# Kernel tuning notes

Measured on AMD Instinct MI355X. Metric: run time of the kernel, lower is better.

Reference implementation:

```python
import jax, jax.numpy as jnp
import numpy as np

# --- module constants (match init_kwargs) ---
DIM = 256
WH, WW = 8, 8            # window_size
H, W = 64, 64            # input_resolution
NUM_HEADS = 1
HEAD_DIM = DIM // NUM_HEADS
SCALE = HEAD_DIM ** -0.5
N = WH * WW
TAB_P = 2 * WW - 1       # a_p/b_p table size (input_resolution != window_size)
TAB_R = 2 * WH - 1


def _relative_coords():
    ch, cw = np.meshgrid(np.arange(WH), np.arange(WW), indexing='ij')
    flat = np.stack([ch.reshape(-1), cw.reshape(-1)])          # (2, N)
    rel = flat[:, :, None] - flat[:, None, :]                  # (2, N, N)
    radius = rel[0]                                            # (N, N) in [-(WH-1), WH-1]
    azimuth = rel[1]                                           # (N, N) in [-(WW-1), WW-1]
    return jnp.asarray(radius, jnp.int32), jnp.asarray(azimuth, jnp.int32)


def setup_inputs() -> dict:
    key = jax.random.key(0)
    ks = jax.random.split(key, 12)
    B_ = 2048
    std = 0.02
    return {
        'x': jax.random.normal(ks[0], (B_, N, DIM), jnp.float32),
        'theta_max': jax.random.uniform(ks[1], (WH,), jnp.float32),
        'qkv_w': jax.random.normal(ks[2], (3 * DIM, DIM), jnp.float32) * (DIM ** -0.5),
        'qkv_b': jnp.zeros((3 * DIM,), jnp.float32),
        'proj_w': jax.random.normal(ks[3], (DIM, DIM), jnp.float32) * (DIM ** -0.5),
        'proj_b': jnp.zeros((DIM,), jnp.float32),
        'a_p': jax.random.normal(ks[4], (TAB_P, NUM_HEADS), jnp.float32) * std,
        'b_p': jax.random.normal(ks[5], (TAB_P, NUM_HEADS), jnp.float32) * std,
        'a_r': jax.random.normal(ks[6], (TAB_R, NUM_HEADS), jnp.float32) * std,
        'b_r': jax.random.normal(ks[7], (TAB_R, NUM_HEADS), jnp.float32) * std,
    }


def reference(x, theta_max, qkv_w, qkv_b, proj_w, proj_b, a_p, b_p, a_r, b_r):
    radius, azimuth = _relative_coords()
    # phi: gather azimuth table (negative indices wrap like torch) + trig bias
    az_idx = jnp.mod(azimuth, TAB_P)
    az_ang = (azimuth.astype(x.dtype) * (2.0 * np.pi / W))[:, :, None]      # (N,N,1)
    A_phi = a_p[az_idx] * jnp.cos(az_ang) + b_p[az_idx] * jnp.sin(az_ang)   # (N,N,h)
    # theta: gather radius table + per-row theta_max scaled trig bias
    r_idx = jnp.mod(radius, TAB_R)
    time_t = N // theta_max.shape[0]
    tmax = jnp.repeat(theta_max, time_t)                                    # (N,)
    r_ang = (radius.astype(x.dtype) * tmax / H)[:, :, None]                 # (N,N,1)
    A_theta = a_r[r_idx] * jnp.cos(r_ang) + b_r[r_idx] * jnp.sin(r_ang)     # (N,N,h)
    bias = jnp.transpose(A_phi + A_theta, (2, 0, 1))[None]                  # (1,h,N,N)

    B_ = x.shape[0]
    qkv = x @ qkv_w.T + qkv_b                                               # (B_,N,3*DIM)
    qkv = qkv.reshape(B_, N, 3, NUM_HEADS, HEAD_DIM).transpose(2, 0, 3, 1, 4)
    q, k, v = qkv[0], qkv[1], qkv[2]                                        # (B_,h,N,hd)
    attn = jnp.einsum('bhnd,bhmd->bhnm', q * SCALE, k) + bias
    attn = jax.nn.softmax(attn, axis=-1)
    out = jnp.einsum('bhnm,bhmd->bhnd', attn, v)                            # (B_,h,N,hd)
    out = out.transpose(0, 2, 1, 3).reshape(B_, N, DIM)
    return out @ proj_w.T + proj_b
```

## Files before the change

### kernel.cpp

```cpp
#include <hip/hip_runtime.h>
#include <hip/hip_bf16.h>


typedef __bf16 bf16x8_t __attribute__((ext_vector_type(8)));
typedef __bf16 bf16x4_t __attribute__((ext_vector_type(4)));
typedef float floatx4_t __attribute__((ext_vector_type(4)));

#define MFMA16(a, b, c) __builtin_amdgcn_mfma_f32_16x16x32_bf16(a, b, c, 0, 0, 0)
#define VPITCH 72

__device__ __forceinline__ void cvt8(const float* src, __bf16* dst) {
  float4 f0 = reinterpret_cast<const float4*>(src)[0];
  float4 f1 = reinterpret_cast<const float4*>(src)[1];
  bf16x8_t h;
  h[0] = (__bf16)f0.x; h[1] = (__bf16)f0.y; h[2] = (__bf16)f0.z; h[3] = (__bf16)f0.w;
  h[4] = (__bf16)f1.x; h[5] = (__bf16)f1.y; h[6] = (__bf16)f1.z; h[7] = (__bf16)f1.w;
  *reinterpret_cast<bf16x8_t*>(dst) = h;
}

__global__ __launch_bounds__(256) void prep_kernel(
    const float* __restrict__ qkv_w, const float* __restrict__ qkv_b,
    const float* __restrict__ proj_w, const float* __restrict__ theta_max,
    const float* __restrict__ a_p, const float* __restrict__ b_p,
    const float* __restrict__ a_r, const float* __restrict__ b_r,
    __bf16* __restrict__ wb, float* __restrict__ bias_ws,
    float* __restrict__ btl) {
  int blk = blockIdx.x, tid = threadIdx.x;
  if (blk < 64) {
    int t = blk * 256 + tid;
    cvt8(&qkv_w[(size_t)t * 8], &wb[(size_t)t * 8]);
  } else if (blk < 80) {
    int t = (blk - 64) * 256 + tid;
    int i = t >> 6, j = t & 63;
    int rad = (i >> 3) - (j >> 3), az = (i & 7) - (j & 7);
    int azm = ((az % 15) + 15) % 15;
    int rdm = ((rad % 15) + 15) % 15;
    float az_ang = (float)az * 0.09817477042468103f;
    float tm = theta_max[j >> 3];
    float r_ang = (float)rad * tm * (1.0f / 64.0f);
    bias_ws[t] = a_p[azm] * cosf(az_ang) + b_p[azm] * sinf(az_ang) +
                 a_r[rdm] * cosf(r_ang) + b_r[rdm] * sinf(r_ang);
  } else {
    int j = blk - 80;
    int k = tid;
    float s = 0.f;
    for (int d = 0; d < 256; ++d)
      s += proj_w[j * 256 + d] * qkv_w[(size_t)(512 + d) * 256 + k];
    wb[(size_t)(512 + j) * 256 + k] = (__bf16)s;
    if (tid == 0) {
      float sb = 0.f;
      for (int d = 0; d < 256; ++d) sb += proj_w[j * 256 + d] * qkv_b[512 + d];
      btl[j] = sb;
    }
  }
}

__global__ __launch_bounds__(256, 1) void fused_kernel(
    const float* __restrict__ x, const __bf16* __restrict__ wb,
    const float* __restrict__ qkv_b, const float* __restrict__ btl,
    const float* __restrict__ bias_ws, const float* __restrict__ proj_b,
    float* __restrict__ out) {
  __shared__ __align__(16) __bf16 ldsX[64 * 256];
  __shared__ __align__(16) __bf16 ldsQ[64 * 256];
  __shared__ __align__(16) __bf16 ldsK[64 * 256];
  __shared__ __align__(16) __bf16 ldsV[256 * 64];
  __shared__ __align__(16) __bf16 ldsP[64 * VPITCH];
  const int b = blockIdx.x;
  const size_t xbase = (size_t)b * 64 * 256;
  const int tid = threadIdx.x;
  const int lane = tid & 63, wave = tid >> 6;
  const int l15 = lane & 15, quad = lane >> 4;

  {
    int m = tid >> 2;
    int u0 = tid & 3;
#pragma unroll
    for (int i = 0; i < 8; ++i) {
      int u = u0 + i * 4;
      __bf16 tmp[8];
      cvt8(&x[xbase + m * 256 + u * 8], tmp);
      *reinterpret_cast<bf16x8_t*>(&ldsX[(m * 32 + (u ^ (m & 7))) * 8]) =
          *reinterpret_cast<bf16x8_t*>(tmp);
    }
  }
  __syncthreads();

#pragma unroll 1
  for (int p = 0; p < 3; ++p) {
    floatx4_t acc[4][4] = {};
#pragma unroll
    for (int kc = 0; kc < 8; ++kc) {
      bf16x8_t af[4], bfr[4];
#pragma unroll
      for (int mt = 0; mt < 4; ++mt)
        af[mt] = *reinterpret_cast<const bf16x8_t*>(
            &ldsX[((mt * 16 + l15) * 32 + ((kc * 4 + quad) ^ (l15 & 7))) * 8]);
#pragma unroll
      for (int ct = 0; ct < 4; ++ct) {
        int n = p * 256 + wave * 64 + ct * 16 + l15;
        bfr[ct] = *reinterpret_cast<const bf16x8_t*>(
            &wb[(size_t)n * 256 + kc * 32 + quad * 8]);
      }
#pragma unroll
      for (int mt = 0; mt < 4; ++mt)
#pragma unroll
        for (int ct = 0; ct < 4; ++ct)
          acc[mt][ct] = MFMA16(af[mt], bfr[ct], acc[mt][ct]);
    }
    if (p < 2) {
      __bf16* dst = (p == 0) ? ldsQ : ldsK;
#pragma unroll
      for (int ct = 0; ct < 4; ++ct) {
        int d = wave * 64 + ct * 16 + l15;
        float bias = qkv_b[p * 256 + d];
        int u = d >> 3;
#pragma unroll
        for (int mt = 0; mt < 4; ++mt)
#pragma unroll
          for (int g = 0; g < 4; ++g) {
            int m = mt * 16 + quad * 4 + g;
            dst[(m * 32 + (u ^ (m & 7))) * 8 + (d & 7)] =
                (__bf16)(acc[mt][ct][g] + bias);
          }
      }
    } else {
#pragma unroll
      for (int ct = 0; ct < 4; ++ct) {
        int d = wave * 64 + ct * 16 + l15;
        float bias = btl[d];
#pragma unroll
        for (int mt = 0; mt < 4; ++mt) {
          bf16x4_t pk;
#pragma unroll
          for (int g = 0; g < 4; ++g) pk[g] = (__bf16)(acc[mt][ct][g] + bias);
          int u = mt * 2 + (quad >> 1);
          *reinterpret_cast<bf16x4_t*>(
              &ldsV[(d * 8 + (u ^ (d & 7))) * 8 + (quad & 1) * 4]) = pk;
        }
      }
    }
    __syncthreads();
  }

  bf16x8_t qf[8];
#pragma unroll
  for (int kc = 0; kc < 8; ++kc)
    qf[kc] = *reinterpret_cast<const bf16x8_t*>(
        &ldsQ[((wave * 16 + l15) * 32 + ((kc * 4 + quad) ^ (l15 & 7))) * 8]);

  floatx4_t accs[4] = {};
#pragma unroll
  for (int ct = 0; ct < 4; ++ct)
#pragma unroll
    for (int kc = 0; kc < 8; ++kc) {
      bf16x8_t bfr = *reinterpret_cast<const bf16x8_t*>(
          &ldsK[((ct * 16 + l15) * 32 + ((kc * 4 + quad) ^ (l15 & 7))) * 8]);
      accs[ct] = MFMA16(qf[kc], bfr, accs[ct]);
    }

  float p[4][4];
#pragma unroll
  for (int ct = 0; ct < 4; ++ct)
#pragma unroll
    for (int g = 0; g < 4; ++g) {
      int row = wave * 16 + quad * 4 + g;
      p[ct][g] = accs[ct][g] * 0.0625f + bias_ws[row * 64 + ct * 16 + l15];
    }
#pragma unroll
  for (int g = 0; g < 4; ++g) {
    float m = fmaxf(fmaxf(p[0][g], p[1][g]), fmaxf(p[2][g], p[3][g]));
#pragma unroll
    for (int off = 1; off < 16; off <<= 1) m = fmaxf(m, __shfl_xor(m, off, 64));
    float l = 0.f;
#pragma unroll
    for (int ct = 0; ct < 4; ++ct) {
      p[ct][g] = __expf(p[ct][g] - m);
      l += p[ct][g];
    }
#pragma unroll
    for (int off = 1; off < 16; off <<= 1) l += __shfl_xor(l, off, 64);
    float inv = 1.0f / l;
    int row = wave * 16 + quad * 4 + g;
#pragma unroll
    for (int ct = 0; ct < 4; ++ct)
      ldsP[row * VPITCH + ct * 16 + l15] = (__bf16)(p[ct][g] * inv);
  }
  __syncthreads();

  floatx4_t acco[16] = {};
#pragma unroll
  for (int kc = 0; kc < 2; ++kc) {
    bf16x8_t af = *reinterpret_cast<const bf16x8_t*>(
        &ldsP[(wave * 16 + l15) * VPITCH + kc * 32 + quad * 8]);
#pragma unroll
    for (int ct = 0; ct < 16; ++ct) {
      int n = ct * 16 + l15;
      bf16x8_t bfr = *reinterpret_cast<const bf16x8_t*>(
          &ldsV[(n * 8 + ((kc * 4 + quad) ^ (n & 7))) * 8]);
      acco[ct] = MFMA16(af, bfr, acco[ct]);
    }
  }

#pragma unroll
  for (int ct = 0; ct < 16; ++ct) {
    int col = ct * 16 + l15;
    float pbv = proj_b[col];
#pragma unroll
    for (int g = 0; g < 4; ++g) {
      int row = wave * 16 + quad * 4 + g;
      out[xbase + (size_t)row * 256 + col] = acco[ct][g] + pbv;
    }
  }
}

extern "C" void kernel_launch(void* const* d_in, const int* in_sizes, int n_in,
                              void* d_out, int out_size, void* d_ws, size_t ws_size,
                              hipStream_t stream) {
  const float* x = (const float*)d_in[0];
  const float* theta_max = (const float*)d_in[1];
  const float* qkv_w = (const float*)d_in[2];
  const float* qkv_b = (const float*)d_in[3];
  const float* proj_w = (const float*)d_in[4];
  const float* proj_b = (const float*)d_in[5];
  const float* a_p = (const float*)d_in[6];
  const float* b_p = (const float*)d_in[7];
  const float* a_r = (const float*)d_in[8];
  const float* b_r = (const float*)d_in[9];
  float* out = (float*)d_out;

  char* ws = (char*)d_ws;
  float* bias_ws = (float*)ws;
  float* btl = (float*)(ws + 16384);
  __bf16* wb = (__bf16*)(ws + 32768);

  hipLaunchKernelGGL(prep_kernel, dim3(336), dim3(256), 0, stream,
                     qkv_w, qkv_b, proj_w, theta_max, a_p, b_p, a_r, b_r,
                     wb, bias_ws, btl);
  hipLaunchKernelGGL(fused_kernel, dim3(2048), dim3(256), 0, stream,
                     x, wb, qkv_b, btl, bias_ws, proj_b, out);
}
```

Measured before the change: 409.9 us.

## Fold Wq^T Wk into single matrix for scores and cut LDS for two blocks per CU

Precomputes M = Wq^T Wk (scaled) plus a key-bias column, so the scores become X·M·X^T instead of separate Q and K projections. The per-window K projection and its LDS buffer are removed, and the V buffer is aliased onto the G buffer. This lowers shared memory enough to allow two blocks per CU via launch bounds. The trade-off is a larger prep kernel, an extra small GEMM against X, and slightly different bf16 rounding. Softmax is also reorganised so each lane owns one query row.

```diff
diff --git a/kernel.cpp b/kernel.cpp
--- a/kernel.cpp
+++ b/kernel.cpp
@@ -23,14 +23,35 @@
     const float* __restrict__ proj_w, const float* __restrict__ theta_max,
     const float* __restrict__ a_p, const float* __restrict__ b_p,
     const float* __restrict__ a_r, const float* __restrict__ b_r,
-    __bf16* __restrict__ wb, float* __restrict__ bias_ws,
-    float* __restrict__ btl) {
+    __bf16* __restrict__ wbM, __bf16* __restrict__ wbV,
+    float* __restrict__ bias_ws, float* __restrict__ btl) {
   int blk = blockIdx.x, tid = threadIdx.x;
-  if (blk < 64) {
-    int t = blk * 256 + tid;
-    cvt8(&qkv_w[(size_t)t * 8], &wb[(size_t)t * 8]);
-  } else if (blk < 80) {
-    int t = (blk - 64) * 256 + tid;
+  if (blk < 256) {
+    int n = blk, k = tid;
+    float s = 0.f;
+    for (int a = 0; a < 256; ++a)
+      s += qkv_w[(size_t)a * 256 + k] * qkv_w[(size_t)(256 + a) * 256 + n];
+    wbM[(size_t)n * 256 + k] = (__bf16)(s * 0.0625f);
+  } else if (blk == 256) {
+    int k = tid;
+    float s = 0.f;
+    for (int a = 0; a < 256; ++a)
+      s += qkv_w[(size_t)(256 + a) * 256 + k] * qkv_b[a];
+    wbM[(size_t)256 * 256 + k] = (__bf16)(s * 0.0625f);
+    for (int r = 257; r < 272; ++r) wbM[(size_t)r * 256 + k] = (__bf16)0.f;
+  } else if (blk < 513) {
+    int j = blk - 257, k = tid;
+    float s = 0.f;
+    for (int d = 0; d < 256; ++d)
+      s += proj_w[j * 256 + d] * qkv_w[(size_t)(512 + d) * 256 + k];
+    wbV[(size_t)j * 256 + k] = (__bf16)s;
+    if (tid == 0) {
+      float sb = 0.f;
+      for (int d = 0; d < 256; ++d) sb += proj_w[j * 256 + d] * qkv_b[512 + d];
+      btl[j] = sb;
+    }
+  } else {
+    int t = (blk - 513) * 256 + tid;
     int i = t >> 6, j = t & 63;
     int rad = (i >> 3) - (j >> 3), az = (i & 7) - (j & 7);
     int azm = ((az % 15) + 15) % 15;
@@ -40,30 +61,16 @@
     float r_ang = (float)rad * tm * (1.0f / 64.0f);
     bias_ws[t] = a_p[azm] * cosf(az_ang) + b_p[azm] * sinf(az_ang) +
                  a_r[rdm] * cosf(r_ang) + b_r[rdm] * sinf(r_ang);
-  } else {
-    int j = blk - 80;
-    int k = tid;
-    float s = 0.f;
-    for (int d = 0; d < 256; ++d)
-      s += proj_w[j * 256 + d] * qkv_w[(size_t)(512 + d) * 256 + k];
-    wb[(size_t)(512 + j) * 256 + k] = (__bf16)s;
-    if (tid == 0) {
-      float sb = 0.f;
-      for (int d = 0; d < 256; ++d) sb += proj_w[j * 256 + d] * qkv_b[512 + d];
-      btl[j] = sb;
-    }
-  }
-}
-
-__global__ __launch_bounds__(256, 1) void fused_kernel(
-    const float* __restrict__ x, const __bf16* __restrict__ wb,
-    const float* __restrict__ qkv_b, const float* __restrict__ btl,
+  }
+}
+
+__global__ __launch_bounds__(256, 2) void fused_kernel(
+    const float* __restrict__ x, const __bf16* __restrict__ wbM,
+    const __bf16* __restrict__ wbV, const float* __restrict__ btl,
     const float* __restrict__ bias_ws, const float* __restrict__ proj_b,
     float* __restrict__ out) {
-  __shared__ __align__(16) __bf16 ldsX[64 * 256];
-  __shared__ __align__(16) __bf16 ldsQ[64 * 256];
-  __shared__ __align__(16) __bf16 ldsK[64 * 256];
-  __shared__ __align__(16) __bf16 ldsV[256 * 64];
+  __shared__ __align__(16) __bf16 ldsX[64 * 32 * 8];
+  __shared__ __align__(16) __bf16 ldsG[64 * 34 * 8];
   __shared__ __align__(16) __bf16 ldsP[64 * VPITCH];
   const int b = blockIdx.x;
   const size_t xbase = (size_t)b * 64 * 256;
@@ -85,9 +92,9 @@
   }
   __syncthreads();
 
-#pragma unroll 1
-  for (int p = 0; p < 3; ++p) {
-    floatx4_t acc[4][4] = {};
+  {
+    floatx4_t accg[4][4] = {};
+    floatx4_t accc[4] = {};
 #pragma unroll
     for (int kc = 0; kc < 8; ++kc) {
       bf16x8_t af[4], bfr[4];
@@ -97,118 +104,163 @@
             &ldsX[((mt * 16 + l15) * 32 + ((kc * 4 + quad) ^ (l15 & 7))) * 8]);
 #pragma unroll
       for (int ct = 0; ct < 4; ++ct) {
-        int n = p * 256 + wave * 64 + ct * 16 + l15;
+        int n = (ct * 4 + wave) * 16 + l15;
         bfr[ct] = *reinterpret_cast<const bf16x8_t*>(
-            &wb[(size_t)n * 256 + kc * 32 + quad * 8]);
+            &wbM[(size_t)n * 256 + kc * 32 + quad * 8]);
       }
 #pragma unroll
       for (int mt = 0; mt < 4; ++mt)
 #pragma unroll
         for (int ct = 0; ct < 4; ++ct)
-          acc[mt][ct] = MFMA16(af[mt], bfr[ct], acc[mt][ct]);
-    }
-    if (p < 2) {
-      __bf16* dst = (p == 0) ? ldsQ : ldsK;
+          accg[mt][ct] = MFMA16(af[mt], bfr[ct], accg[mt][ct]);
+      if (wave == 0) {
+        bf16x8_t bc = *reinterpret_cast<const bf16x8_t*>(
+            &wbM[(size_t)(256 + l15) * 256 + kc * 32 + quad * 8]);
+#pragma unroll
+        for (int mt = 0; mt < 4; ++mt) accc[mt] = MFMA16(af[mt], bc, accc[mt]);
+      }
+    }
+#pragma unroll
+    for (int ct = 0; ct < 4; ++ct) {
+      int n0 = (ct * 4 + wave) * 16 + l15;
+      int u = n0 >> 3;
+#pragma unroll
+      for (int mt = 0; mt < 4; ++mt)
+#pragma unroll
+        for (int g = 0; g < 4; ++g) {
+          int m = mt * 16 + quad * 4 + g;
+          ldsG[(m * 34 + (u ^ (m & 7))) * 8 + (n0 & 7)] =
+              (__bf16)accg[mt][ct][g];
+        }
+    }
+    if (wave == 0) {
+      int n0 = 256 + l15;
+      int u = 32 + (l15 >> 3);
+#pragma unroll
+      for (int mt = 0; mt < 4; ++mt)
+#pragma unroll
+        for (int g = 0; g < 4; ++g) {
+          int m = mt * 16 + quad * 4 + g;
+          ldsG[(m * 34 + u) * 8 + (n0 & 7)] = (__bf16)accc[mt][g];
+        }
+    }
+  }
+  __syncthreads();
+
+  floatx4_t accs[4] = {};
+#pragma unroll
+  for (int kc = 0; kc < 8; ++kc) {
+    bf16x8_t af[4];
+#pragma unroll
+    for (int mt = 0; mt < 4; ++mt)
+      af[mt] = *reinterpret_cast<const bf16x8_t*>(
+          &ldsX[((mt * 16 + l15) * 32 + ((kc * 4 + quad) ^ (l15 & 7))) * 8]);
+    int r = wave * 16 + l15;
+    bf16x8_t bfr = *reinterpret_cast<const bf16x8_t*>(
+        &ldsG[(r * 34 + ((kc * 4 + quad) ^ (r & 7))) * 8]);
+#pragma unroll
+    for (int mt = 0; mt < 4; ++mt) accs[mt] = MFMA16(af[mt], bfr, accs[mt]);
+  }
+
+  {
+    const int i = wave * 16 + l15;
+    float p[4][4];
+    float mx = -1e30f;
+#pragma unroll
+    for (int mt = 0; mt < 4; ++mt)
+#pragma unroll
+      for (int g = 0; g < 4; ++g) {
+        int j = mt * 16 + quad * 4 + g;
+        float cj = (float)ldsG[(j * 34 + 32) * 8];
+        p[mt][g] = accs[mt][g] + bias_ws[i * 64 + j] + cj;
+        mx = fmaxf(mx, p[mt][g]);
+      }
+    mx = fmaxf(mx, __shfl_xor(mx, 16, 64));
+    mx = fmaxf(mx, __shfl_xor(mx, 32, 64));
+    float l = 0.f;
+#pragma unroll
+    for (int mt = 0; mt < 4; ++mt)
+#pragma unroll
+      for (int g = 0; g < 4; ++g) {
+        p[mt][g] = __expf(p[mt][g] - mx);
+        l += p[mt][g];
+      }
+    l += __shfl_xor(l, 16, 64);
+    l += __shfl_xor(l, 32, 64);
+    float inv = 1.0f / l;
+#pragma unroll
+    for (int mt = 0; mt < 4; ++mt)
+#pragma unroll
+      for (int g = 0; g < 4; ++g) {
+        int j = mt * 16 + quad * 4 + g;
+        ldsP[i * VPITCH + j] = (__bf16)(p[mt][g] * inv);
+      }
+  }
+  __syncthreads();
+
+  {
+    __bf16* ldsV = ldsG;
+    floatx4_t accv[4][4] = {};
+#pragma unroll
+    for (int kc = 0; kc < 8; ++kc) {
+      bf16x8_t af[4], bfr[4];
+#pragma unroll
+      for (int mt = 0; mt < 4; ++mt)
+        af[mt] = *reinterpret_cast<const bf16x8_t*>(
+            &ldsX[((mt * 16 + l15) * 32 + ((kc * 4 + quad) ^ (l15 & 7))) * 8]);
 #pragma unroll
       for (int ct = 0; ct < 4; ++ct) {
-        int d = wave * 64 + ct * 16 + l15;
-        float bias = qkv_b[p * 256 + d];
-        int u = d >> 3;
-#pragma unroll
-        for (int mt = 0; mt < 4; ++mt)
-#pragma unroll
-          for (int g = 0; g < 4; ++g) {
-            int m = mt * 16 + quad * 4 + g;
-            dst[(m * 32 + (u ^ (m & 7))) * 8 + (d & 7)] =
-                (__bf16)(acc[mt][ct][g] + bias);
-          }
-      }
-    } else {
-#pragma unroll
-      for (int ct = 0; ct < 4; ++ct) {
-        int d = wave * 64 + ct * 16 + l15;
-        float bias = btl[d];
-#pragma unroll
-        for (int mt = 0; mt < 4; ++mt) {
-          bf16x4_t pk;
-#pragma unroll
-          for (int g = 0; g < 4; ++g) pk[g] = (__bf16)(acc[mt][ct][g] + bias);
-          int u = mt * 2 + (quad >> 1);
-          *reinterpret_cast<bf16x4_t*>(
-              &ldsV[(d * 8 + (u ^ (d & 7))) * 8 + (quad & 1) * 4]) = pk;
-        }
-      }
-    }
-    __syncthreads();
-  }
-
-  bf16x8_t qf[8];
-#pragma unroll
-  for (int kc = 0; kc < 8; ++kc)
-    qf[kc] = *reinterpret_cast<const bf16x8_t*>(
-        &ldsQ[((wave * 16 + l15) * 32 + ((kc * 4 + quad) ^ (l15 & 7))) * 8]);
-
-  floatx4_t accs[4] = {};
-#pragma unroll
-  for (int ct = 0; ct < 4; ++ct)
-#pragma unroll
-    for (int kc = 0; kc < 8; ++kc) {
-      bf16x8_t bfr = *reinterpret_cast<const bf16x8_t*>(
-          &ldsK[((ct * 16 + l15) * 32 + ((kc * 4 + quad) ^ (l15 & 7))) * 8]);
-      accs[ct] = MFMA16(qf[kc], bfr, accs[ct]);
-    }
-
-  float p[4][4];
-#pragma unroll
-  for (int ct = 0; ct < 4; ++ct)
-#pragma unroll
-    for (int g = 0; g < 4; ++g) {
-      int row = wave * 16 + quad * 4 + g;
-      p[ct][g] = accs[ct][g] * 0.0625f + bias_ws[row * 64 + ct * 16 + l15];
-    }
-#pragma unroll
-  for (int g = 0; g < 4; ++g) {
-    float m = fmaxf(fmaxf(p[0][g], p[1][g]), fmaxf(p[2][g], p[3][g]));
-#pragma unroll
-    for (int off = 1; off < 16; off <<= 1) m = fmaxf(m, __shfl_xor(m, off, 64));
-    float l = 0.f;
+        int n = wave * 64 + ct * 16 + l15;
+        bfr[ct] = *reinterpret_cast<const bf16x8_t*>(
+            &wbV[(size_t)n * 256 + kc * 32 + quad * 8]);
+      }
+#pragma unroll
+      for (int mt = 0; mt < 4; ++mt)
+#pragma unroll
+        for (int ct = 0; ct < 4; ++ct)
+          accv[mt][ct] = MFMA16(af[mt], bfr[ct], accv[mt][ct]);
+    }
 #pragma unroll
     for (int ct = 0; ct < 4; ++ct) {
-      p[ct][g] = __expf(p[ct][g] - m);
-      l += p[ct][g];
-    }
-#pragma unroll
-    for (int off = 1; off < 16; off <<= 1) l += __shfl_xor(l, off, 64);
-    float inv = 1.0f / l;
-    int row = wave * 16 + quad * 4 + g;
-#pragma unroll
-    for (int ct = 0; ct < 4; ++ct)
-      ldsP[row * VPITCH + ct * 16 + l15] = (__bf16)(p[ct][g] * inv);
-  }
-  __syncthreads();
-
-  floatx4_t acco[16] = {};
-#pragma unroll
-  for (int kc = 0; kc < 2; ++kc) {
-    bf16x8_t af = *reinterpret_cast<const bf16x8_t*>(
-        &ldsP[(wave * 16 + l15) * VPITCH + kc * 32 + quad * 8]);
+      int d = wave * 64 + ct * 16 + l15;
+      float bias = btl[d];
+#pragma unroll
+      for (int mt = 0; mt < 4; ++mt) {
+        bf16x4_t pk;
+#pragma unroll
+        for (int g = 0; g < 4; ++g) pk[g] = (__bf16)(accv[mt][ct][g] + bias);
+        int u = mt * 2 + (quad >> 1);
+        *reinterpret_cast<bf16x4_t*>(
+            &ldsV[(d * 8 + (u ^ (d & 7))) * 8 + (quad & 1) * 4]) = pk;
+      }
+    }
+  }
+  __syncthreads();
+
+  {
+    const __bf16* ldsV = ldsG;
+    floatx4_t acco[16] = {};
+#pragma unroll
+    for (int kc = 0; kc < 2; ++kc) {
+      bf16x8_t af = *reinterpret_cast<const bf16x8_t*>(
+          &ldsP[(wave * 16 + l15) * VPITCH + kc * 32 + quad * 8]);
+#pragma unroll
+      for (int ct = 0; ct < 16; ++ct) {
+        int n = ct * 16 + l15;
+        bf16x8_t bfr = *reinterpret_cast<const bf16x8_t*>(
+            &ldsV[(n * 8 + ((kc * 4 + quad) ^ (n & 7))) * 8]);
+        acco[ct] = MFMA16(af, bfr, acco[ct]);
+      }
+    }
 #pragma unroll
     for (int ct = 0; ct < 16; ++ct) {
-      int n = ct * 16 + l15;
-      bf16x8_t bfr = *reinterpret_cast<const bf16x8_t*>(
-          &ldsV[(n * 8 + ((kc * 4 + quad) ^ (n & 7))) * 8]);
-      acco[ct] = MFMA16(af, bfr, acco[ct]);
-    }
-  }
-
-#pragma unroll
-  for (int ct = 0; ct < 16; ++ct) {
-    int col = ct * 16 + l15;
-    float pbv = proj_b[col];
-#pragma unroll
-    for (int g = 0; g < 4; ++g) {
-      int row = wave * 16 + quad * 4 + g;
-      out[xbase + (size_t)row * 256 + col] = acco[ct][g] + pbv;
+      int col = ct * 16 + l15;
+      float pbv = proj_b[col];
+#pragma unroll
+      for (int g = 0; g < 4; ++g) {
+        int row = wave * 16 + quad * 4 + g;
+        out[xbase + (size_t)row * 256 + col] = acco[ct][g] + pbv;
+      }
     }
   }
 }
@@ -231,11 +283,12 @@
   char* ws = (char*)d_ws;
   float* bias_ws = (float*)ws;
   float* btl = (float*)(ws + 16384);
-  __bf16* wb = (__bf16*)(ws + 32768);
-
-  hipLaunchKernelGGL(prep_kernel, dim3(336), dim3(256), 0, stream,
+  __bf16* wbM = (__bf16*)(ws + 32768);
+  __bf16* wbV = (__bf16*)(ws + 172032);
+
+  hipLaunchKernelGGL(prep_kernel, dim3(529), dim3(256), 0, stream,
                      qkv_w, qkv_b, proj_w, theta_max, a_p, b_p, a_r, b_r,
-                     wb, bias_ws, btl);
+                     wbM, wbV, bias_ws, btl);
   hipLaunchKernelGGL(fused_kernel, dim3(2048), dim3(256), 0, stream,
-                     x, wb, qkv_b, btl, bias_ws, proj_b, out);
-}
+                     x, wbM, wbV, btl, bias_ws, proj_b, out);
+}
```

Measured after the change: 337.9 us. -17.6%, faster.
